# Kernel tuning notes

Hardware: AMD Instinct MI355X
Metric: run time of the kernel (lower is better)

## Reference

```python
import jax, jax.numpy as jnp
import numpy as np

NUM_VARIABLES = 20
NUM_LAYERS = 3
NUM_CONSTRAINTS = 64
NUM_STATES = 2 ** NUM_VARIABLES
TOP_K = 10  # min(10, num_states)


def _state_bits():
    # bits[i, v] = v-th bit of i, MSB first (matches format(i, '0{n}b'))
    idx = jnp.arange(NUM_STATES, dtype=jnp.int32)
    shifts = jnp.arange(NUM_VARIABLES - 1, -1, -1, dtype=jnp.int32)
    return ((idx[:, None] >> shifts[None, :]) & 1).astype(jnp.float32)


def setup_inputs() -> dict:
    key = jax.random.key(0)
    k1, k2, k3 = jax.random.split(key, 3)
    return {
        "problem_constraints": jax.random.normal(k1, (NUM_CONSTRAINTS, NUM_VARIABLES), dtype=jnp.float32),
        "beta_params": jax.random.normal(k2, (NUM_LAYERS,), dtype=jnp.float32) * 0.1,
        "gamma_params": jax.random.normal(k3, (NUM_LAYERS,), dtype=jnp.float32) * 0.1,
    }


def reference(problem_constraints, beta_params, gamma_params):
    bits = _state_bits()  # [S, n]
    # cost_function evaluated on every basis state (vectorized over 2^n states)
    viol = bits @ problem_constraints.T  # [S, C]
    costs = jnp.sum(jnp.maximum(viol - 1.0, 0.0) ** 2, axis=1) + 0.1 * jnp.sum(bits, axis=1)
    costs = jax.lax.stop_gradient(costs)  # torch fills costs via .item(), detaching them

    amps = jnp.full((NUM_STATES,), 1.0 / np.sqrt(NUM_STATES), dtype=jnp.float32)
    for layer in range(NUM_LAYERS):
        # problem unitary: exp(-i*gamma*cost) applied to real amps, then cast back
        # to float32 (torch .to(float) keeps the real part) => multiply by cos.
        amps = amps * jnp.cos(gamma_params[layer] * costs)
        # mixer: mixed[i] = amps[i] + 0.1*sin(beta) * sum_bit amps[i ^ (1<<bit)]
        grid = amps.reshape((2,) * NUM_VARIABLES)
        nb = jnp.zeros_like(grid)
        for ax in range(NUM_VARIABLES):  # structural loop over qubit axes
            nb = nb + jnp.flip(grid, axis=ax)
        mixed = amps + 0.1 * jnp.sin(beta_params[layer]) * nb.reshape(-1)
        amps = mixed / jnp.linalg.norm(mixed)

    probs = amps ** 2  # |amplitude|^2 (amps are real after the casts)
    _, top_idx = jax.lax.top_k(probs, TOP_K)
    top_assignments = bits[top_idx]  # [K, n]
    assignment_costs = costs[top_idx]  # same formula as cost_function on each
    best = jnp.argmin(assignment_costs)
    optimal_assignment = top_assignments[best]
    optimal_cost = assignment_costs[best]
    return (optimal_assignment, optimal_cost, probs, top_assignments, assignment_costs)
```

## Files before the change

kernel.cpp:

```cpp
#include <hip/hip_runtime.h>
#include <math.h>

#define NV 20
#define NC 64
#define NSTATES (1u << 20)
#define TOPK 10
#define NB1 256
#define NCAND (NB1 * TOPK)

__global__ __launch_bounds__(256) void k_costs(const float* __restrict__ C,
                                               float* __restrict__ costs,
                                               float* __restrict__ ph0,
                                               const float* __restrict__ gamma,
                                               double* __restrict__ scal,
                                               unsigned* __restrict__ ctr) {
    __shared__ float CT[17][NC];
    __shared__ float lowT[8][NC];
    const int tid = threadIdx.x;

    if (blockIdx.x == 0) {
        if (tid < 8) scal[tid] = 0.0;
        if (tid == 8) *ctr = 0u;
    }

    for (int e = tid; e < 17 * NC; e += 256) {
        int k = e / NC, c = e % NC;
        CT[k][c] = C[c * NV + (16 - k)];
    }
    for (int e = tid; e < 8 * NC; e += 256) {
        int m = e >> 6, c = e & 63;
        float v = 0.0f;
        if (m & 1) v += C[c * NV + 19];
        if (m & 2) v += C[c * NV + 18];
        if (m & 4) v += C[c * NV + 17];
        lowT[m][c] = v;
    }
    __syncthreads();

    unsigned t = blockIdx.x * 256u + (unsigned)tid;
    float g0 = gamma[0];

    float cost[8];
    #pragma unroll
    for (int s = 0; s < 8; ++s)
        cost[s] = 0.1f * (float)__popc(t * 8u + (unsigned)s);

    #pragma unroll
    for (int cc = 0; cc < 4; ++cc) {
        float4 bb[4];
        #pragma unroll
        for (int q = 0; q < 4; ++q) bb[q] = make_float4(-1.f, -1.f, -1.f, -1.f);
        #pragma unroll
        for (int k = 0; k < 17; ++k) {
            float bf = (float)((t >> k) & 1u);
            const float4* row = ((const float4*)(&CT[k][0])) + 4 * cc;
            #pragma unroll
            for (int q = 0; q < 4; ++q) {
                float4 cv = row[q];
                bb[q].x = fmaf(bf, cv.x, bb[q].x);
                bb[q].y = fmaf(bf, cv.y, bb[q].y);
                bb[q].z = fmaf(bf, cv.z, bb[q].z);
                bb[q].w = fmaf(bf, cv.w, bb[q].w);
            }
        }
        #pragma unroll
        for (int s = 0; s < 8; ++s) {
            const float4* lrow = ((const float4*)(&lowT[s][0])) + 4 * cc;
            #pragma unroll
            for (int q = 0; q < 4; ++q) {
                float4 lv = lrow[q];
                float4 v;
                v.x = bb[q].x + lv.x; v.y = bb[q].y + lv.y;
                v.z = bb[q].z + lv.z; v.w = bb[q].w + lv.w;
                float r;
                r = fmaxf(v.x, 0.f); cost[s] = fmaf(r, r, cost[s]);
                r = fmaxf(v.y, 0.f); cost[s] = fmaf(r, r, cost[s]);
                r = fmaxf(v.z, 0.f); cost[s] = fmaf(r, r, cost[s]);
                r = fmaxf(v.w, 0.f); cost[s] = fmaf(r, r, cost[s]);
            }
        }
    }

    float4* co = (float4*)(costs + (size_t)t * 8u);
    co[0] = make_float4(cost[0], cost[1], cost[2], cost[3]);
    co[1] = make_float4(cost[4], cost[5], cost[6], cost[7]);
    float ph[8];
    #pragma unroll
    for (int s = 0; s < 8; ++s) ph[s] = 0x1p-10f * cosf(g0 * cost[s]);
    float4* po = (float4*)(ph0 + (size_t)t * 8u);
    po[0] = make_float4(ph[0], ph[1], ph[2], ph[3]);
    po[1] = make_float4(ph[4], ph[5], ph[6], ph[7]);
}

template <int LAYER, bool ALIN, bool ALOUT>
__global__ __launch_bounds__(1024, 4) void k_mix(const float* __restrict__ pin,
                                                 const float* __restrict__ costs,
                                                 float* __restrict__ pout,
                                                 const float* __restrict__ gamma,
                                                 const float* __restrict__ beta,
                                                 double* __restrict__ scal) {
    __shared__ float4 tile[1024];
    __shared__ double dpart[16];
    const unsigned lq = threadIdx.x;
    const unsigned i4 = blockIdx.x * 1024u + lq;
    float s = 0.1f * sinf(beta[LAYER]);
    float prevscale = (LAYER == 0) ? 1.0f : (float)(1.0 / sqrt(scal[LAYER - 1]));

    auto ld4 = [&](unsigned j4) -> float4 {
        if (ALIN) return ((const float4*)pin)[j4];
        float4 a;
        a.x = pin[4u * j4 + 0]; a.y = pin[4u * j4 + 1];
        a.z = pin[4u * j4 + 2]; a.w = pin[4u * j4 + 3];
        return a;
    };

    float4 own = ld4(i4);
    tile[lq] = own;

    float4 gv[4];
    #pragma unroll
    for (int u = 0; u < 4; ++u) gv[u] = ld4(i4 ^ (1u << (17 - u)));

    __syncthreads();

    float4 nb = make_float4(0.f, 0.f, 0.f, 0.f);
    #pragma unroll
    for (int u = 0; u < 4; ++u) {
        nb.x += gv[u].x; nb.y += gv[u].y; nb.z += gv[u].z; nb.w += gv[u].w;
    }
    #pragma unroll
    for (int u = 0; u < 4; ++u) gv[u] = ld4(i4 ^ (1u << (13 - u)));
    #pragma unroll
    for (int u = 0; u < 4; ++u) {
        nb.x += gv[u].x; nb.y += gv[u].y; nb.z += gv[u].z; nb.w += gv[u].w;
    }
    #pragma unroll
    for (int p = 11; p >= 2; --p) {
        float4 v = tile[lq ^ (1u << (p - 2))];
        nb.x += v.x; nb.y += v.y; nb.z += v.z; nb.w += v.w;
    }
    nb.x += own.z; nb.y += own.w; nb.z += own.x; nb.w += own.y;
    nb.x += own.y; nb.y += own.x; nb.z += own.w; nb.w += own.z;

    float4 m;
    m.x = prevscale * fmaf(s, nb.x, own.x);
    m.y = prevscale * fmaf(s, nb.y, own.y);
    m.z = prevscale * fmaf(s, nb.z, own.z);
    m.w = prevscale * fmaf(s, nb.w, own.w);

    float4 o;
    if (LAYER < 2) {
        float gn = gamma[LAYER + 1];
        float4 c = ((const float4*)costs)[i4];
        o.x = m.x * cosf(gn * c.x);
        o.y = m.y * cosf(gn * c.y);
        o.z = m.z * cosf(gn * c.z);
        o.w = m.w * cosf(gn * c.w);
    } else {
        o = m;
    }
    if (ALOUT) {
        ((float4*)pout)[i4] = o;
    } else {
        pout[4u * i4 + 0] = o.x; pout[4u * i4 + 1] = o.y;
        pout[4u * i4 + 2] = o.z; pout[4u * i4 + 3] = o.w;
    }

    double ss = (double)m.x * m.x + (double)m.y * m.y +
                (double)m.z * m.z + (double)m.w * m.w;
    #pragma unroll
    for (int off = 32; off > 0; off >>= 1) ss += __shfl_down(ss, off);
    int wid = threadIdx.x >> 6;
    if ((threadIdx.x & 63) == 0) dpart[wid] = ss;
    __syncthreads();
    if (threadIdx.x == 0) {
        double tt = 0.0;
        #pragma unroll
        for (int w = 0; w < 16; ++w) tt += dpart[w];
        atomicAdd(&scal[LAYER], tt);
    }
}

template <bool ALIN>
__global__ __launch_bounds__(256) void k_ptop(const float* __restrict__ A,
                                              const double* __restrict__ scal2,
                                              const float* __restrict__ costs,
                                              float* __restrict__ out,
                                              unsigned long long* __restrict__ cand,
                                              unsigned* __restrict__ ctr) {
    __shared__ unsigned long long warr[4];
    __shared__ int lastblk;
    __shared__ unsigned topi[TOPK];
    __shared__ float topc[TOPK];
    const int tid = threadIdx.x;
    float* probs_out = out + 21;
    unsigned b4 = blockIdx.x * 1024u;
    float scale = (float)(1.0 / sqrt(*scal2));

    unsigned long long k[16];
    #pragma unroll
    for (int u = 0; u < 4; ++u) {
        unsigned j4 = b4 + (unsigned)tid + 256u * u;
        float4 v;
        if (ALIN) v = ((const float4*)A)[j4];
        else {
            v.x = A[4u * j4 + 0]; v.y = A[4u * j4 + 1];
            v.z = A[4u * j4 + 2]; v.w = A[4u * j4 + 3];
        }
        float4 p;
        p.x = v.x * scale; p.x *= p.x;
        p.y = v.y * scale; p.y *= p.y;
        p.z = v.z * scale; p.z *= p.z;
        p.w = v.w * scale; p.w *= p.w;
        unsigned e0 = 4u * j4;
        probs_out[e0 + 0] = p.x; probs_out[e0 + 1] = p.y;
        probs_out[e0 + 2] = p.z; probs_out[e0 + 3] = p.w;
        k[4 * u + 0] = ((unsigned long long)__float_as_uint(p.x) << 32) | (unsigned long long)(0xFFFFFFFFu - (e0 + 0));
        k[4 * u + 1] = ((unsigned long long)__float_as_uint(p.y) << 32) | (unsigned long long)(0xFFFFFFFFu - (e0 + 1));
        k[4 * u + 2] = ((unsigned long long)__float_as_uint(p.z) << 32) | (unsigned long long)(0xFFFFFFFFu - (e0 + 2));
        k[4 * u + 3] = ((unsigned long long)__float_as_uint(p.w) << 32) | (unsigned long long)(0xFFFFFFFFu - (e0 + 3));
    }

    for (int r = 0; r < TOPK; ++r) {
        unsigned long long loc = 0ull;
        #pragma unroll
        for (int j = 0; j < 16; ++j) if (k[j] > loc) loc = k[j];
        #pragma unroll
        for (int off = 32; off > 0; off >>= 1) {
            unsigned long long o = __shfl_down(loc, off);
            if (o > loc) loc = o;
        }
        if ((tid & 63) == 0) warr[tid >> 6] = loc;
        __syncthreads();
        unsigned long long win = warr[0];
        if (warr[1] > win) win = warr[1];
        if (warr[2] > win) win = warr[2];
        if (warr[3] > win) win = warr[3];
        __syncthreads();
        #pragma unroll
        for (int j = 0; j < 16; ++j) if (k[j] == win) k[j] = 0ull;
        if (tid == 0) cand[blockIdx.x * TOPK + r] = win;
    }

    __threadfence();
    if (tid == 0) {
        unsigned old = atomicAdd(ctr, 1u);
        lastblk = (old == NB1 - 1) ? 1 : 0;
    }
    __syncthreads();
    if (!lastblk) return;
    __threadfence();

    unsigned long long c2[TOPK];
    #pragma unroll
    for (int u = 0; u < TOPK; ++u) c2[u] = cand[tid + 256 * u];

    for (int r = 0; r < TOPK; ++r) {
        unsigned long long loc = 0ull;
        #pragma unroll
        for (int u = 0; u < TOPK; ++u) if (c2[u] > loc) loc = c2[u];
        #pragma unroll
        for (int off = 32; off > 0; off >>= 1) {
            unsigned long long o = __shfl_down(loc, off);
            if (o > loc) loc = o;
        }
        if ((tid & 63) == 0) warr[tid >> 6] = loc;
        __syncthreads();
        unsigned long long win = warr[0];
        if (warr[1] > win) win = warr[1];
        if (warr[2] > win) win = warr[2];
        if (warr[3] > win) win = warr[3];
        __syncthreads();
        #pragma unroll
        for (int u = 0; u < TOPK; ++u) if (c2[u] == win) c2[u] = 0ull;
        if (tid == 0) topi[r] = 0xFFFFFFFFu - (unsigned)(win & 0xFFFFFFFFull);
        __syncthreads();
    }

    const unsigned S = NSTATES;
    if (tid < TOPK * NV) {
        int kk = tid / NV, vv = tid % NV;
        out[21 + S + (unsigned)tid] = (float)((topi[kk] >> (NV - 1 - vv)) & 1u);
    }
    if (tid < TOPK) {
        float c = costs[topi[tid]];
        topc[tid] = c;
        out[21 + S + TOPK * NV + (unsigned)tid] = c;
    }
    __syncthreads();
    if (tid == 0) {
        int best = 0;
        for (int kk = 1; kk < TOPK; ++kk)
            if (topc[kk] < topc[best]) best = kk;
        unsigned gi = topi[best];
        for (int vv = 0; vv < NV; ++vv)
            out[vv] = (float)((gi >> (NV - 1 - vv)) & 1u);
        out[NV] = topc[best];
    }
}

extern "C" void kernel_launch(void* const* d_in, const int* in_sizes, int n_in,
                              void* d_out_, int out_size, void* d_ws, size_t ws_size,
                              hipStream_t stream) {
    (void)in_sizes; (void)n_in; (void)out_size;
    const float* C     = (const float*)d_in[0];
    const float* beta  = (const float*)d_in[1];
    const float* gamma = (const float*)d_in[2];
    float* out = (float*)d_out_;
    char* ws = (char*)d_ws;
    const size_t S4 = (size_t)NSTATES * sizeof(float);

    double* scal = (double*)ws;
    unsigned* ctr = (unsigned*)(ws + 64);
    unsigned long long* cand = (unsigned long long*)(ws + 1024);
    float* costs = (float*)(ws + 32768);
    float* A     = (float*)(ws + 32768 + S4);
    const size_t need_full = 32768 + 3 * S4;
    bool wsbig = (ws_size >= need_full);
    float* B = wsbig ? (float*)(ws + 32768 + 2 * S4) : (out + 21);

    k_costs<<<512, 256, 0, stream>>>(C, costs, A, gamma, scal, ctr);

    if (wsbig) {
        k_mix<0, true, true ><<<256, 1024, 0, stream>>>(A, costs, B, gamma, beta, scal);
        k_mix<1, true, true ><<<256, 1024, 0, stream>>>(B, costs, A, gamma, beta, scal);
        k_mix<2, true, true ><<<256, 1024, 0, stream>>>(A, costs, B, gamma, beta, scal);
        k_ptop<true ><<<NB1, 256, 0, stream>>>(B, scal + 2, costs, out, cand, ctr);
    } else {
        k_mix<0, true, false><<<256, 1024, 0, stream>>>(A, costs, B, gamma, beta, scal);
        k_mix<1, false, true><<<256, 1024, 0, stream>>>(B, costs, A, gamma, beta, scal);
        k_mix<2, true, false><<<256, 1024, 0, stream>>>(A, costs, B, gamma, beta, scal);
        k_ptop<false><<<NB1, 256, 0, stream>>>(B, scal + 2, costs, out, cand, ctr);
    }
}
```

Measured before the change: 91.02 us.

## Diagonalize mixer with Walsh-Hadamard transforms and defer normalization

Replaces the per-layer neighbour-sum mixer with a forward Walsh-Hadamard transform, an eigenvalue scaling by 1+s(20-2·popcount), and an inverse transform, split into row (LDS, 12 bits) and column (6 bits plus in-register) passes. The cost phases are fused into the row passes, and the norm is computed once at the end instead of per layer. This removes the strided neighbour gathers but adds more kernel launches, more full-array passes and many barrier-separated LDS butterfly stages.

```diff
diff --git a/kernel.cpp b/kernel.cpp
--- a/kernel.cpp
+++ b/kernel.cpp
@@ -8,177 +8,260 @@
 #define NB1 256
 #define NCAND (NB1 * TOPK)
 
-__global__ __launch_bounds__(256) void k_costs(const float* __restrict__ C,
-                                               float* __restrict__ costs,
-                                               float* __restrict__ ph0,
-                                               const float* __restrict__ gamma,
-                                               double* __restrict__ scal,
-                                               unsigned* __restrict__ ctr) {
-    __shared__ float CT[17][NC];
-    __shared__ float lowT[8][NC];
-    const int tid = threadIdx.x;
-
-    if (blockIdx.x == 0) {
-        if (tid < 8) scal[tid] = 0.0;
-        if (tid == 8) *ctr = 0u;
-    }
-
-    for (int e = tid; e < 17 * NC; e += 256) {
-        int k = e / NC, c = e % NC;
-        CT[k][c] = C[c * NV + (16 - k)];
-    }
-    for (int e = tid; e < 8 * NC; e += 256) {
-        int m = e >> 6, c = e & 63;
-        float v = 0.0f;
-        if (m & 1) v += C[c * NV + 19];
-        if (m & 2) v += C[c * NV + 18];
-        if (m & 4) v += C[c * NV + 17];
-        lowT[m][c] = v;
-    }
-    __syncthreads();
-
-    unsigned t = blockIdx.x * 256u + (unsigned)tid;
-    float g0 = gamma[0];
-
-    float cost[8];
-    #pragma unroll
-    for (int s = 0; s < 8; ++s)
-        cost[s] = 0.1f * (float)__popc(t * 8u + (unsigned)s);
-
-    #pragma unroll
-    for (int cc = 0; cc < 4; ++cc) {
-        float4 bb[4];
-        #pragma unroll
-        for (int q = 0; q < 4; ++q) bb[q] = make_float4(-1.f, -1.f, -1.f, -1.f);
-        #pragma unroll
-        for (int k = 0; k < 17; ++k) {
-            float bf = (float)((t >> k) & 1u);
-            const float4* row = ((const float4*)(&CT[k][0])) + 4 * cc;
-            #pragma unroll
-            for (int q = 0; q < 4; ++q) {
-                float4 cv = row[q];
-                bb[q].x = fmaf(bf, cv.x, bb[q].x);
-                bb[q].y = fmaf(bf, cv.y, bb[q].y);
-                bb[q].z = fmaf(bf, cv.z, bb[q].z);
-                bb[q].w = fmaf(bf, cv.w, bb[q].w);
-            }
-        }
-        #pragma unroll
-        for (int s = 0; s < 8; ++s) {
-            const float4* lrow = ((const float4*)(&lowT[s][0])) + 4 * cc;
-            #pragma unroll
-            for (int q = 0; q < 4; ++q) {
-                float4 lv = lrow[q];
-                float4 v;
-                v.x = bb[q].x + lv.x; v.y = bb[q].y + lv.y;
-                v.z = bb[q].z + lv.z; v.w = bb[q].w + lv.w;
-                float r;
-                r = fmaxf(v.x, 0.f); cost[s] = fmaf(r, r, cost[s]);
-                r = fmaxf(v.y, 0.f); cost[s] = fmaf(r, r, cost[s]);
-                r = fmaxf(v.z, 0.f); cost[s] = fmaf(r, r, cost[s]);
-                r = fmaxf(v.w, 0.f); cost[s] = fmaf(r, r, cost[s]);
-            }
-        }
-    }
-
-    float4* co = (float4*)(costs + (size_t)t * 8u);
-    co[0] = make_float4(cost[0], cost[1], cost[2], cost[3]);
-    co[1] = make_float4(cost[4], cost[5], cost[6], cost[7]);
-    float ph[8];
-    #pragma unroll
-    for (int s = 0; s < 8; ++s) ph[s] = 0x1p-10f * cosf(g0 * cost[s]);
-    float4* po = (float4*)(ph0 + (size_t)t * 8u);
-    po[0] = make_float4(ph[0], ph[1], ph[2], ph[3]);
-    po[1] = make_float4(ph[4], ph[5], ph[6], ph[7]);
-}
-
-template <int LAYER, bool ALIN, bool ALOUT>
-__global__ __launch_bounds__(1024, 4) void k_mix(const float* __restrict__ pin,
-                                                 const float* __restrict__ costs,
-                                                 float* __restrict__ pout,
-                                                 const float* __restrict__ gamma,
-                                                 const float* __restrict__ beta,
-                                                 double* __restrict__ scal) {
-    __shared__ float4 tile[1024];
-    __shared__ double dpart[16];
-    const unsigned lq = threadIdx.x;
-    const unsigned i4 = blockIdx.x * 1024u + lq;
-    float s = 0.1f * sinf(beta[LAYER]);
-    float prevscale = (LAYER == 0) ? 1.0f : (float)(1.0 / sqrt(scal[LAYER - 1]));
-
-    auto ld4 = [&](unsigned j4) -> float4 {
-        if (ALIN) return ((const float4*)pin)[j4];
-        float4 a;
-        a.x = pin[4u * j4 + 0]; a.y = pin[4u * j4 + 1];
-        a.z = pin[4u * j4 + 2]; a.w = pin[4u * j4 + 3];
-        return a;
-    };
-
-    float4 own = ld4(i4);
-    tile[lq] = own;
-
-    float4 gv[4];
-    #pragma unroll
-    for (int u = 0; u < 4; ++u) gv[u] = ld4(i4 ^ (1u << (17 - u)));
-
-    __syncthreads();
-
-    float4 nb = make_float4(0.f, 0.f, 0.f, 0.f);
-    #pragma unroll
-    for (int u = 0; u < 4; ++u) {
-        nb.x += gv[u].x; nb.y += gv[u].y; nb.z += gv[u].z; nb.w += gv[u].w;
-    }
-    #pragma unroll
-    for (int u = 0; u < 4; ++u) gv[u] = ld4(i4 ^ (1u << (13 - u)));
-    #pragma unroll
-    for (int u = 0; u < 4; ++u) {
-        nb.x += gv[u].x; nb.y += gv[u].y; nb.z += gv[u].z; nb.w += gv[u].w;
-    }
-    #pragma unroll
-    for (int p = 11; p >= 2; --p) {
-        float4 v = tile[lq ^ (1u << (p - 2))];
-        nb.x += v.x; nb.y += v.y; nb.z += v.z; nb.w += v.w;
-    }
-    nb.x += own.z; nb.y += own.w; nb.z += own.x; nb.w += own.y;
-    nb.x += own.y; nb.y += own.x; nb.z += own.w; nb.w += own.z;
-
-    float4 m;
-    m.x = prevscale * fmaf(s, nb.x, own.x);
-    m.y = prevscale * fmaf(s, nb.y, own.y);
-    m.z = prevscale * fmaf(s, nb.z, own.z);
-    m.w = prevscale * fmaf(s, nb.w, own.w);
-
+
+__device__ __forceinline__ float4 wht4(float4 v) {
+  float a0 = v.x + v.y, a1 = v.x - v.y, a2 = v.z + v.w, a3 = v.z - v.w;
+  float4 r;
+  r.x = a0 + a2; r.y = a1 + a3; r.z = a0 - a2; r.w = a1 - a3;
+  return r;
+}
+
+__device__ __forceinline__ float4 wht_lds10(float4 v, int tid,
+                                            float4* b0, float4* b1, int& sel) {
+  #pragma unroll
+  for (int st = 0; st < 10; ++st) {
+    float4* b = sel ? b1 : b0; sel ^= 1;
+    b[tid] = v;
+    __syncthreads();
+    float4 p = b[tid ^ (1 << st)];
+    if (((tid >> st) & 1) == 0) {
+      v.x += p.x; v.y += p.y; v.z += p.z; v.w += p.w;
+    } else {
+      v.x = p.x - v.x; v.y = p.y - v.y; v.z = p.z - v.z; v.w = p.w - v.w;
+    }
+  }
+  return v;
+}
+
+__global__ __launch_bounds__(1024) void k_costs_wht(const float* __restrict__ C,
+                                                    float* __restrict__ costs,
+                                                    float* __restrict__ A,
+                                                    const float* __restrict__ gamma,
+                                                    double* __restrict__ scal,
+                                                    unsigned* __restrict__ ctr) {
+  __shared__ float CT[17][NC];
+  __shared__ float lowT[8][NC];
+  __shared__ float4 rb0[1024], rb1[1024];
+  const int tid = threadIdx.x;
+  const unsigned t = blockIdx.x * 1024u + (unsigned)tid;
+
+  if (blockIdx.x == 0) {
+    if (tid < 8) scal[tid] = 0.0;
+    if (tid == 8) *ctr = 0u;
+  }
+
+  for (int e = tid; e < 17 * NC; e += 1024) {
+    int k = e / NC, c = e % NC;
+    CT[k][c] = C[c * NV + (16 - k)];
+  }
+  for (int e = tid; e < 8 * NC; e += 1024) {
+    int m = e >> 6, c = e & 63;
+    float v = 0.0f;
+    if (m & 1) v += C[c * NV + 19];
+    if (m & 2) v += C[c * NV + 18];
+    if (m & 4) v += C[c * NV + 17];
+    lowT[m][c] = v;
+  }
+  __syncthreads();
+
+  float cost[4];
+  #pragma unroll
+  for (int s = 0; s < 4; ++s)
+    cost[s] = 0.1f * (float)__popc(4u * t + (unsigned)s);
+  const int m01 = (int)((t & 1u) << 2);
+
+  #pragma unroll
+  for (int cc = 0; cc < 4; ++cc) {
+    float4 bb[4];
+    #pragma unroll
+    for (int q = 0; q < 4; ++q) bb[q] = make_float4(-1.f, -1.f, -1.f, -1.f);
+    #pragma unroll
+    for (int k = 0; k < 17; ++k) {
+      float bf = (float)((t >> (k + 1)) & 1u);
+      const float4* row = ((const float4*)(&CT[k][0])) + 4 * cc;
+      #pragma unroll
+      for (int q = 0; q < 4; ++q) {
+        float4 cv = row[q];
+        bb[q].x = fmaf(bf, cv.x, bb[q].x);
+        bb[q].y = fmaf(bf, cv.y, bb[q].y);
+        bb[q].z = fmaf(bf, cv.z, bb[q].z);
+        bb[q].w = fmaf(bf, cv.w, bb[q].w);
+      }
+    }
+    #pragma unroll
+    for (int s = 0; s < 4; ++s) {
+      const float4* lrow = ((const float4*)(&lowT[m01 | s][0])) + 4 * cc;
+      #pragma unroll
+      for (int q = 0; q < 4; ++q) {
+        float4 lv = lrow[q];
+        float4 v;
+        v.x = bb[q].x + lv.x; v.y = bb[q].y + lv.y;
+        v.z = bb[q].z + lv.z; v.w = bb[q].w + lv.w;
+        float r;
+        r = fmaxf(v.x, 0.f); cost[s] = fmaf(r, r, cost[s]);
+        r = fmaxf(v.y, 0.f); cost[s] = fmaf(r, r, cost[s]);
+        r = fmaxf(v.z, 0.f); cost[s] = fmaf(r, r, cost[s]);
+        r = fmaxf(v.w, 0.f); cost[s] = fmaf(r, r, cost[s]);
+      }
+    }
+  }
+
+  ((float4*)costs)[t] = make_float4(cost[0], cost[1], cost[2], cost[3]);
+
+  float g0 = gamma[0];
+  float4 v;
+  v.x = 0x1p-10f * cosf(g0 * cost[0]);
+  v.y = 0x1p-10f * cosf(g0 * cost[1]);
+  v.z = 0x1p-10f * cosf(g0 * cost[2]);
+  v.w = 0x1p-10f * cosf(g0 * cost[3]);
+
+  v = wht4(v);
+  int sel = 0;
+  v = wht_lds10(v, tid, rb0, rb1, sel);
+  ((float4*)A)[t] = v;
+}
+
+__global__ __launch_bounds__(1024) void k_col(float* __restrict__ A,
+                                              const float* __restrict__ beta,
+                                              int layer) {
+  __shared__ float w0[256 * 17];
+  __shared__ float w1[256 * 17];
+  const int tid = threadIdx.x;
+  const unsigned c0 = blockIdx.x * 16u;
+  const float s = 0.1f * sinf(beta[layer]);
+
+  const int lr = tid >> 2, cq = tid & 3;
+  const size_t gq = (size_t)lr * 1024 + (c0 >> 2) + (unsigned)cq;
+  float4 v4 = ((const float4*)A)[gq];
+  w0[lr * 17 + cq * 4 + 0] = v4.x;
+  w0[lr * 17 + cq * 4 + 1] = v4.y;
+  w0[lr * 17 + cq * 4 + 2] = v4.z;
+  w0[lr * 17 + cq * 4 + 3] = v4.w;
+  __syncthreads();
+
+  const int br = tid >> 4, col = tid & 15;
+  float v[4];
+  #pragma unroll
+  for (int k = 0; k < 4; ++k) v[k] = w0[(br + 64 * k) * 17 + col];
+  int sel = 1;
+
+  #pragma unroll
+  for (int st = 0; st < 6; ++st) {
+    float* b = sel ? w1 : w0; sel ^= 1;
+    #pragma unroll
+    for (int k = 0; k < 4; ++k) b[(br + 64 * k) * 17 + col] = v[k];
+    __syncthreads();
+    float p[4];
+    #pragma unroll
+    for (int k = 0; k < 4; ++k) p[k] = b[((br ^ (1 << st)) + 64 * k) * 17 + col];
+    if (((br >> st) & 1) == 0) {
+      #pragma unroll
+      for (int k = 0; k < 4; ++k) v[k] += p[k];
+    } else {
+      #pragma unroll
+      for (int k = 0; k < 4; ++k) v[k] = p[k] - v[k];
+    }
+  }
+  {
+    float n0 = v[0] + v[1], n1 = v[0] - v[1], n2 = v[2] + v[3], n3 = v[2] - v[3];
+    v[0] = n0 + n2; v[1] = n1 + n3; v[2] = n0 - n2; v[3] = n1 - n3;
+  }
+  const int popl = __popc(c0 | (unsigned)col);
+  #pragma unroll
+  for (int k = 0; k < 4; ++k) {
+    int lam = 20 - 2 * (__popc((unsigned)(br + 64 * k)) + popl);
+    v[k] *= (1.0f + s * (float)lam) * 0x1p-8f;
+  }
+  {
+    float n0 = v[0] + v[1], n1 = v[0] - v[1], n2 = v[2] + v[3], n3 = v[2] - v[3];
+    v[0] = n0 + n2; v[1] = n1 + n3; v[2] = n0 - n2; v[3] = n1 - n3;
+  }
+  #pragma unroll
+  for (int st = 0; st < 6; ++st) {
+    float* b = sel ? w1 : w0; sel ^= 1;
+    #pragma unroll
+    for (int k = 0; k < 4; ++k) b[(br + 64 * k) * 17 + col] = v[k];
+    __syncthreads();
+    float p[4];
+    #pragma unroll
+    for (int k = 0; k < 4; ++k) p[k] = b[((br ^ (1 << st)) + 64 * k) * 17 + col];
+    if (((br >> st) & 1) == 0) {
+      #pragma unroll
+      for (int k = 0; k < 4; ++k) v[k] += p[k];
+    } else {
+      #pragma unroll
+      for (int k = 0; k < 4; ++k) v[k] = p[k] - v[k];
+    }
+  }
+  {
+    float* b = sel ? w1 : w0;
+    #pragma unroll
+    for (int k = 0; k < 4; ++k) b[(br + 64 * k) * 17 + col] = v[k];
+    __syncthreads();
     float4 o;
-    if (LAYER < 2) {
-        float gn = gamma[LAYER + 1];
-        float4 c = ((const float4*)costs)[i4];
-        o.x = m.x * cosf(gn * c.x);
-        o.y = m.y * cosf(gn * c.y);
-        o.z = m.z * cosf(gn * c.z);
-        o.w = m.w * cosf(gn * c.w);
-    } else {
-        o = m;
-    }
-    if (ALOUT) {
-        ((float4*)pout)[i4] = o;
-    } else {
-        pout[4u * i4 + 0] = o.x; pout[4u * i4 + 1] = o.y;
-        pout[4u * i4 + 2] = o.z; pout[4u * i4 + 3] = o.w;
-    }
-
-    double ss = (double)m.x * m.x + (double)m.y * m.y +
-                (double)m.z * m.z + (double)m.w * m.w;
-    #pragma unroll
-    for (int off = 32; off > 0; off >>= 1) ss += __shfl_down(ss, off);
-    int wid = threadIdx.x >> 6;
-    if ((threadIdx.x & 63) == 0) dpart[wid] = ss;
-    __syncthreads();
-    if (threadIdx.x == 0) {
-        double tt = 0.0;
-        #pragma unroll
-        for (int w = 0; w < 16; ++w) tt += dpart[w];
-        atomicAdd(&scal[LAYER], tt);
-    }
+    o.x = b[lr * 17 + cq * 4 + 0];
+    o.y = b[lr * 17 + cq * 4 + 1];
+    o.z = b[lr * 17 + cq * 4 + 2];
+    o.w = b[lr * 17 + cq * 4 + 3];
+    ((float4*)A)[gq] = o;
+  }
+}
+
+__global__ __launch_bounds__(1024) void k_row_mid(float* __restrict__ A,
+                                                  const float* __restrict__ costs,
+                                                  const float* __restrict__ gamma,
+                                                  int gi) {
+  __shared__ float4 rb0[1024], rb1[1024];
+  const int tid = threadIdx.x;
+  const size_t q = (size_t)blockIdx.x * 1024 + tid;
+  float4 v = ((const float4*)A)[q];
+  int sel = 0;
+  v = wht4(v);
+  v = wht_lds10(v, tid, rb0, rb1, sel);
+  const float g = gamma[gi];
+  float4 c = ((const float4*)costs)[q];
+  v.x = v.x * 0x1p-12f * cosf(g * c.x);
+  v.y = v.y * 0x1p-12f * cosf(g * c.y);
+  v.z = v.z * 0x1p-12f * cosf(g * c.z);
+  v.w = v.w * 0x1p-12f * cosf(g * c.w);
+  v = wht4(v);
+  v = wht_lds10(v, tid, rb0, rb1, sel);
+  ((float4*)A)[q] = v;
+}
+
+template <bool AL>
+__global__ __launch_bounds__(1024) void k_row_fin(const float* __restrict__ A,
+                                                  float* __restrict__ B,
+                                                  double* __restrict__ scal) {
+  __shared__ float4 rb0[1024], rb1[1024];
+  __shared__ double dpart[16];
+  const int tid = threadIdx.x;
+  const size_t q = (size_t)blockIdx.x * 1024 + tid;
+  float4 v = ((const float4*)A)[q];
+  int sel = 0;
+  v = wht4(v);
+  v = wht_lds10(v, tid, rb0, rb1, sel);
+  v.x *= 0x1p-12f; v.y *= 0x1p-12f; v.z *= 0x1p-12f; v.w *= 0x1p-12f;
+
+  if (AL) {
+    ((float4*)B)[q] = v;
+  } else {
+    B[4 * q + 0] = v.x; B[4 * q + 1] = v.y;
+    B[4 * q + 2] = v.z; B[4 * q + 3] = v.w;
+  }
+
+  double ss = (double)v.x * v.x + (double)v.y * v.y +
+              (double)v.z * v.z + (double)v.w * v.w;
+  #pragma unroll
+  for (int off = 32; off > 0; off >>= 1) ss += __shfl_down(ss, off);
+  if ((tid & 63) == 0) dpart[tid >> 6] = ss;
+  __syncthreads();
+  if (tid == 0) {
+    double tt = 0.0;
+    #pragma unroll
+    for (int w = 0; w < 16; ++w) tt += dpart[w];
+    atomicAdd(&scal[0], tt);
+  }
 }
 
 template <bool ALIN>
@@ -319,17 +402,17 @@
     bool wsbig = (ws_size >= need_full);
     float* B = wsbig ? (float*)(ws + 32768 + 2 * S4) : (out + 21);
 
-    k_costs<<<512, 256, 0, stream>>>(C, costs, A, gamma, scal, ctr);
-
+    k_costs_wht<<<256, 1024, 0, stream>>>(C, costs, A, gamma, scal, ctr);
+    k_col     <<<256, 1024, 0, stream>>>(A, beta, 0);
+    k_row_mid <<<256, 1024, 0, stream>>>(A, costs, gamma, 1);
+    k_col     <<<256, 1024, 0, stream>>>(A, beta, 1);
+    k_row_mid <<<256, 1024, 0, stream>>>(A, costs, gamma, 2);
+    k_col     <<<256, 1024, 0, stream>>>(A, beta, 2);
     if (wsbig) {
-        k_mix<0, true, true ><<<256, 1024, 0, stream>>>(A, costs, B, gamma, beta, scal);
-        k_mix<1, true, true ><<<256, 1024, 0, stream>>>(B, costs, A, gamma, beta, scal);
-        k_mix<2, true, true ><<<256, 1024, 0, stream>>>(A, costs, B, gamma, beta, scal);
-        k_ptop<true ><<<NB1, 256, 0, stream>>>(B, scal + 2, costs, out, cand, ctr);
+        k_row_fin<true ><<<256, 1024, 0, stream>>>(A, B, scal);
+        k_ptop<true ><<<NB1, 256, 0, stream>>>(B, scal, costs, out, cand, ctr);
     } else {
-        k_mix<0, true, false><<<256, 1024, 0, stream>>>(A, costs, B, gamma, beta, scal);
-        k_mix<1, false, true><<<256, 1024, 0, stream>>>(B, costs, A, gamma, beta, scal);
-        k_mix<2, true, false><<<256, 1024, 0, stream>>>(A, costs, B, gamma, beta, scal);
-        k_ptop<false><<<NB1, 256, 0, stream>>>(B, scal + 2, costs, out, cand, ctr);
-    }
-}
+        k_row_fin<false><<<256, 1024, 0, stream>>>(A, B, scal);
+        k_ptop<false><<<NB1, 256, 0, stream>>>(B, scal, costs, out, cand, ctr);
+    }
+}
```

New measurement: 110.6 us. 21.5% more time.
